# Optimization experiments

Hardware: AMD Instinct MI355X
Metric: run time of the kernel (lower is better)

## Reference

```python
import jax, jax.numpy as jnp
import numpy as np

NUM_HEADS = 8
NUM_CLS = 1
WINDOW = 4          # one-sided window radius
DILATION = 2
THETA = 10000.0
COORD_HIGH = 100000.0


def _rotate_half(t):
    # [..., x1, x2, ...] -> [..., -x2, x1, ...]
    x1 = t[..., 0::2]
    x2 = t[..., 1::2]
    return jnp.stack([-x2, x1], axis=-1).reshape(t.shape)


def _rope2d(t, coords):
    # t: (B, H, L, D), coords: (B, L, 2)
    head_dim = t.shape[-1]
    half = head_dim // 2
    inv_freq = 1.0 / (THETA ** (jnp.arange(0, half, 2, dtype=jnp.float32) / half))  # (half//2,)
    xy = coords.astype(jnp.float32) / COORD_HIGH                                    # (B, L, 2)
    fx = xy[..., 0][..., None] * inv_freq                                           # (B, L, half//2)
    fy = xy[..., 1][..., None] * inv_freq
    fx = jnp.repeat(fx, 2, axis=-1)                                                 # (B, L, half)
    fy = jnp.repeat(fy, 2, axis=-1)
    freqs = jnp.concatenate([fx, fy], axis=-1)                                      # (B, L, D)
    cos = jnp.cos(freqs)[:, None]                                                   # (B, 1, L, D)
    sin = jnp.sin(freqs)[:, None]
    return t * cos + _rotate_half(t) * sin


def setup_inputs() -> dict:
    key = jax.random.key(0)
    k1, k2, k3, k4 = jax.random.split(key, 4)
    B, L, E = 2, 8192, 512
    S = NUM_CLS + L
    x = jax.random.normal(k1, (B, S, E), dtype=jnp.float32)
    coords = jax.random.randint(k2, (B, L, 2), 0, 100000, dtype=jnp.int32)
    w_qkv = jax.random.normal(k3, (3 * E, E), dtype=jnp.float32) * 0.02
    b_qkv = jnp.zeros((3 * E,), dtype=jnp.float32)
    w_out = jax.random.normal(k4, (E, E), dtype=jnp.float32) * 0.02
    b_out = jnp.zeros((E,), dtype=jnp.float32)
    return {"x": x, "coords": coords, "w_qkv": w_qkv, "b_qkv": b_qkv,
            "w_out": w_out, "b_out": b_out}


def reference(x, coords, w_qkv, b_qkv, w_out, b_out):
    B, S, E = x.shape
    H = NUM_HEADS
    D = E // H
    L = S - NUM_CLS
    scale = 1.0 / np.sqrt(D).astype(np.float32)

    qkv = x @ w_qkv.T + b_qkv                                  # (B, S, 3E)
    qkv = qkv.reshape(B, S, 3, H, D).transpose(2, 0, 3, 1, 4)  # (3, B, H, S, D)
    q, k, v = qkv[0], qkv[1], qkv[2]

    # 2D RoPE on patch tokens only
    q = jnp.concatenate([q[:, :, :NUM_CLS], _rope2d(q[:, :, NUM_CLS:], coords)], axis=2)
    k = jnp.concatenate([k[:, :, :NUM_CLS], _rope2d(k[:, :, NUM_CLS:], coords)], axis=2)

    # ---- global CLS queries attend to all tokens ----
    s_cls = jnp.einsum('bhqd,bhkd->bhqk', q[:, :, :NUM_CLS], k) * scale
    cls_out = jnp.einsum('bhqk,bhkd->bhqd', jax.nn.softmax(s_cls, axis=-1), v)

    # ---- patch queries: CLS keys + dilated local window ----
    q_p = q[:, :, NUM_CLS:]
    k_p, v_p = k[:, :, NUM_CLS:], v[:, :, NUM_CLS:]
    k_cls, v_cls = k[:, :, :NUM_CLS], v[:, :, :NUM_CLS]

    pad = WINDOW * DILATION
    W = 2 * WINDOW + 1
    kp = jnp.pad(k_p, ((0, 0), (0, 0), (pad, pad), (0, 0)))
    vp = jnp.pad(v_p, ((0, 0), (0, 0), (pad, pad), (0, 0)))

    pos = jnp.arange(L)
    offsets = jnp.arange(W) * DILATION
    gidx = pos[:, None] + offsets[None, :]                     # (L, W), indices into padded seq
    kw = jnp.take(kp, gidx, axis=2)                            # (B, H, L, W, D)
    vw = jnp.take(vp, gidx, axis=2)

    win_pos = (jnp.arange(W) - WINDOW) * DILATION
    in_bounds = (pos[:, None] + win_pos >= 0) & (pos[:, None] + win_pos < L)  # (L, W)

    s_win = jnp.einsum('bhld,bhlwd->bhlw', q_p, kw) * scale
    s_win = jnp.where(in_bounds, s_win, -jnp.inf)
    s_c = jnp.einsum('bhld,bhcd->bhlc', q_p, k_cls) * scale
    attn = jax.nn.softmax(jnp.concatenate([s_c, s_win], axis=-1), axis=-1)  # (B,H,L,C+W)

    patch_out = (jnp.einsum('bhlc,bhcd->bhld', attn[..., :NUM_CLS], v_cls)
                 + jnp.einsum('bhlw,bhlwd->bhld', attn[..., NUM_CLS:], vw))

    out = jnp.concatenate([cls_out, patch_out], axis=2)        # (B, H, S, D)
    out = out.transpose(0, 2, 1, 3).reshape(B, S, E)
    return out @ w_out.T + b_out
```

## Files before the change

### kernel.cpp

```cpp
#include <hip/hip_runtime.h>
#include <math.h>

#define B_ 2
#define S_ 8193
#define L_ 8192
#define E_ 512
#define H_ 8
#define D_ 64
#define QKV_COLS 1536
#define SCALE 0.125f
#define M_ROWS 16386
#define M_PAD 16512

typedef unsigned short u16;
typedef __attribute__((ext_vector_type(8))) short bf16x8;
typedef __attribute__((ext_vector_type(8))) unsigned short u16x8;
typedef __attribute__((ext_vector_type(4))) float f32x4;

__device__ __forceinline__ u16 f2bf(float f) {
    unsigned u = __float_as_uint(f);
    unsigned r = (u + 0x7fffu + ((u >> 16) & 1u)) >> 16;
    return (u16)r;
}
__device__ __forceinline__ float bf2f(u16 h) {
    return __uint_as_float((unsigned)h << 16);
}

__device__ __forceinline__ void gload_lds16(const void* g, void* l) {
    __builtin_amdgcn_global_load_lds(
        (const __attribute__((address_space(1))) void*)g,
        (__attribute__((address_space(3))) void*)l, 16, 0, 0);
}

#define WAITV0() asm volatile("s_waitcnt vmcnt(0)" ::: "memory")
#define BAR()    __builtin_amdgcn_s_barrier()

#define PREP_W0 (M_PAD * E_ / 4)
#define PREP_W1 (QKV_COLS * E_ / 4)
#define PREP_W2 (E_ * E_ / 4)
#define PREP_W3 (B_ * L_ * 32)
#define PREP_W4 ((M_PAD - M_ROWS) * E_ / 8)
#define PREP_TOTAL (PREP_W0 + PREP_W1 + PREP_W2 + PREP_W3 + PREP_W4)

__global__ __launch_bounds__(256) void prep_kernel(
    const float* __restrict__ x,
    const float* __restrict__ w_qkv, const float* __restrict__ w_out,
    const int* __restrict__ coords,
    u16* __restrict__ xb, u16* __restrict__ wqb, u16* __restrict__ wob,
    float2* __restrict__ tab, u16* __restrict__ attnb)
{
    long i = (long)blockIdx.x * 256 + threadIdx.x;
    if (i < PREP_W0) {
        const long row = i >> 7;
        ushort4 o = make_ushort4(0, 0, 0, 0);
        if (row < M_ROWS) {
            const float4 v = *(const float4*)(x + i * 4);
            o.x = f2bf(v.x); o.y = f2bf(v.y); o.z = f2bf(v.z); o.w = f2bf(v.w);
        }
        *(ushort4*)(xb + i * 4) = o;
        return;
    }
    i -= PREP_W0;
    if (i < PREP_W1) {
        const float4 v = *(const float4*)(w_qkv + i * 4);
        ushort4 o = { f2bf(v.x), f2bf(v.y), f2bf(v.z), f2bf(v.w) };
        *(ushort4*)(wqb + i * 4) = o;
        return;
    }
    i -= PREP_W1;
    if (i < PREP_W2) {
        const float4 v = *(const float4*)(w_out + i * 4);
        ushort4 o = { f2bf(v.x), f2bf(v.y), f2bf(v.z), f2bf(v.w) };
        *(ushort4*)(wob + i * 4) = o;
        return;
    }
    i -= PREP_W2;
    if (i < PREP_W3) {
        const int p2 = (int)i & 31;
        const int bl = (int)i >> 5;
        const float coord = (float)coords[(size_t)bl * 2 + (p2 >> 4)] * 1e-5f;
        const float inv = exp2f(-0.83048202372184f * (float)(p2 & 15));
        float sn, cs;
        __sincosf(coord * inv, &sn, &cs);
        tab[i] = make_float2(cs, sn);
        return;
    }
    i -= PREP_W3;
    if (i < PREP_W4) {
        u16x8 z = {};
        *(u16x8*)(attnb + (size_t)M_ROWS * E_ + i * 8) = z;
    }
}

template <int MODE>
__global__ __launch_bounds__(512, 6) void gemm512(
    const u16* __restrict__ A, const u16* __restrict__ W,
    const float* __restrict__ bias, void* __restrict__ Cv,
    const float2* __restrict__ tab, int M, int N)
{
    __shared__ __align__(16) u16 smem[16384];

    const int nwg = gridDim.x * gridDim.y;
    const int orig = blockIdx.y * gridDim.x + blockIdx.x;
    const int qq = nwg >> 3, rr = nwg & 7;
    const int xcd = orig & 7, off = orig >> 3;
    const int wgid = (xcd < rr ? xcd * (qq + 1) : rr * (qq + 1) + (xcd - rr) * qq) + off;
    const int m0 = (wgid / gridDim.x) * 128;
    const int n0 = (wgid % gridDim.x) * 128;

    const int tid  = threadIdx.x;
    const int wid  = tid >> 6;
    const int lane = tid & 63;
    const int wm = (wid >> 2) * 64;
    const int wn = (wid & 3) * 32;
    const int fr = lane & 15;
    const int fq = lane >> 4;
    const int sfq = (fq ^ ((fr >> 1) & 3)) * 8;

    const int arow = tid >> 2;
    const int agch = ((tid & 3) ^ ((arow >> 1) & 3)) * 8;
    const u16* ga = A + (size_t)(m0 + arow) * 512 + agch;
    const u16* gw = W + (size_t)(n0 + arow) * 512 + agch;

    f32x4 acc[4][2] = {};

    #define STAGE(rb, kt)                                                       \
        do {                                                                    \
            gload_lds16(ga + (kt) * 32, smem + (rb) * 4096 + wid * 512);        \
            gload_lds16(gw + (kt) * 32, smem + 8192 + (rb) * 4096 + wid * 512); \
        } while (0)

    #define COMPUTE(rb)                                                         \
        do {                                                                    \
            const u16* as_ = smem + (rb) * 4096;                                \
            const u16* bs_ = smem + 8192 + (rb) * 4096;                         \
            bf16x8 a[4], b[2];                                                  \
            _Pragma("unroll")                                                   \
            for (int mi = 0; mi < 4; ++mi)                                      \
                a[mi] = *(const bf16x8*)(as_ + (wm + mi * 16 + fr) * 32 + sfq); \
            _Pragma("unroll")                                                   \
            for (int ni = 0; ni < 2; ++ni)                                      \
                b[ni] = *(const bf16x8*)(bs_ + (wn + ni * 16 + fr) * 32 + sfq); \
            _Pragma("unroll")                                                   \
            for (int mi = 0; mi < 4; ++mi)                                      \
                _Pragma("unroll")                                               \
                for (int ni = 0; ni < 2; ++ni)                                  \
                    acc[mi][ni] = __builtin_amdgcn_mfma_f32_16x16x32_bf16(      \
                        a[mi], b[ni], acc[mi][ni], 0, 0, 0);                    \
        } while (0)

    STAGE(0, 0);

    for (int t = 0; t < 16; ++t) {
        WAITV0();
        BAR();
        if (t + 1 < 16) STAGE((t + 1) & 1, t + 1);
        COMPUTE(t & 1);
    }

    #undef STAGE
    #undef COMPUTE

    __syncthreads();

    if (MODE == 1) {
        u16* st = smem;
        const bool rope_blk = (n0 < 2 * E_);
        #pragma unroll
        for (int mi = 0; mi < 4; ++mi) {
            #pragma unroll
            for (int j = 0; j < 4; ++j) {
                const int row = wm + mi * 16 + fq * 4 + j;
                const int gm = m0 + row;
                int b = 0, s = gm;
                if (gm >= S_) { b = 1; s = gm - S_; }
                const bool rot = rope_blk && (gm < M) && (s > 0);
                const float2* trow = tab + ((size_t)(b * L_ + (s - 1)) << 5);
                #pragma unroll
                for (int ni = 0; ni < 2; ++ni) {
                    const int col = wn + ni * 16 + fr;
                    const int gn = n0 + col;
                    float v = acc[mi][ni][j] + bias[gn];
                    const float partner = __shfl_xor(v, 1, 64);
                    if (rot) {
                        const float2 tt = trow[(gn & 63) >> 1];
                        v = (gn & 1) ? (v * tt.x + partner * tt.y)
                                     : (v * tt.x - partner * tt.y);
                    }
                    st[row * 128 + col] = f2bf(v);
                }
            }
        }
        __syncthreads();
        u16* C = (u16*)Cv;
        #pragma unroll
        for (int i = 0; i < 4; ++i) {
            const int slot = i * 512 + tid;
            const int row = slot >> 4;
            const int coff = (slot & 15) * 8;
            const int gm = m0 + row;
            if (gm < M)
                *(u16x8*)(C + (size_t)gm * N + n0 + coff) =
                    *(const u16x8*)(st + row * 128 + coff);
        }
    } else {
        float* stf = (float*)smem;
        float* C = (float*)Cv;
        #pragma unroll
        for (int h = 0; h < 2; ++h) {
            if ((wid >> 2) == h) {
                #pragma unroll
                for (int mi = 0; mi < 4; ++mi)
                    #pragma unroll
                    for (int j = 0; j < 4; ++j) {
                        const int lrow = mi * 16 + fq * 4 + j;
                        #pragma unroll
                        for (int ni = 0; ni < 2; ++ni) {
                            const int col = wn + ni * 16 + fr;
                            stf[lrow * 128 + col] = acc[mi][ni][j] + bias[n0 + col];
                        }
                    }
            }
            __syncthreads();
            #pragma unroll
            for (int i = 0; i < 4; ++i) {
                const int slot = i * 512 + tid;
                const int row = slot >> 5;
                const int coff = (slot & 31) * 4;
                const int gm = m0 + h * 64 + row;
                if (gm < M)
                    *(float4*)(C + (size_t)gm * N + n0 + coff) =
                        *(const float4*)(stf + row * 128 + coff);
            }
            __syncthreads();
        }
    }
}

#define NCHUNK 64
#define CLS_ROWS 129
#define CLS_BLOCKS (B_ * H_ * NCHUNK)
#define PQT 256
#define PATCH_BLOCKS (B_ * H_ * (L_ / PQT))

__global__ __launch_bounds__(256) void attn_fused(
    const u16* __restrict__ qkvb, float* __restrict__ part,
    u16* __restrict__ attnb)
{
    __shared__ __align__(16) u16 sbuf[272 * 64];
    __shared__ float kcvc[128];
    __shared__ float sm4[4], sl4[4];

    const int blk = blockIdx.x;

    if (blk < CLS_BLOCKS) {
        const int bh = blk >> 6, ch = blk & 63;
        const int b = bh >> 3, h = bh & 7;
        const int wid = threadIdx.x >> 6, lane = threadIdx.x & 63;
        const size_t base = (size_t)b * S_ * QKV_COLS;

        const float q = bf2f(qkvb[base + h * D_ + lane]);

        const int lo = ch * CLS_ROWS;
        const int hi = (lo + CLS_ROWS < S_) ? lo + CLS_ROWS : S_;

        float m = -1e30f, lsum = 0.f, acc = 0.f;
        for (int j = lo + wid; j < hi; j += 4) {
            const size_t roff = base + (size_t)j * QKV_COLS;
            float t = q * bf2f(qkvb[roff + E_ + h * D_ + lane]);
            #pragma unroll
            for (int o = 32; o; o >>= 1) t += __shfl_xor(t, o, 64);
            t *= SCALE;
            const float mn = fmaxf(m, t);
            const float corr = __expf(m - mn);
            const float p = __expf(t - mn);
            lsum = lsum * corr + p;
            acc = acc * corr + p * bf2f(qkvb[roff + 2 * E_ + h * D_ + lane]);
            m = mn;
        }

        float* sacc = (float*)sbuf;
        if (lane == 0) { sm4[wid] = m; sl4[wid] = lsum; }
        sacc[wid * 64 + lane] = acc;
        __syncthreads();
        if (wid == 0) {
            const float gm = fmaxf(fmaxf(sm4[0], sm4[1]), fmaxf(sm4[2], sm4[3]));
            float gl = 0.f, ga = 0.f;
            #pragma unroll
            for (int w = 0; w < 4; ++w) {
                const float c = __expf(sm4[w] - gm);
                gl += sl4[w] * c;
                ga += sacc[w * 64 + lane] * c;
            }
            float* pp = part + ((size_t)bh * NCHUNK + ch) * 66;
            if (lane == 0) { pp[0] = gm; pp[1] = gl; }
            pp[2 + lane] = ga;
        }
        return;
    }

    const int pblk = blk - CLS_BLOCKS;
    const int qt = pblk & 31;
    const int h = (pblk >> 5) & 7;
    const int b = pblk >> 8;
    const int l0 = qt * PQT;
    const size_t base = (size_t)b * S_ * QKV_COLS;
    const int hoff = h * D_;

    u16* kv = sbuf;
    float* kc = kcvc;
    float* vc = kcvc + 64;

    const int t = threadIdx.x;

    if (t < 64) kc[t] = bf2f(qkvb[base + E_ + hoff + t]);
    else if (t < 128) vc[t - 64] = bf2f(qkvb[base + 2 * E_ + hoff + (t - 64)]);

    #pragma unroll
    for (int i = 0; i < 9; ++i) {
        const int s = i * 256 + t;
        if (s < 272 * 8) {
            const int r = s >> 3, c = s & 7;
            const int lg = l0 - 8 + r;
            u16x8 v = {};
            if (lg >= 0 && lg < L_)
                v = *(const u16x8*)(qkvb + base + (size_t)(1 + lg) * QKV_COLS + E_ + hoff + c * 8);
            *(u16x8*)(kv + r * 64 + ((c ^ (r & 7)) * 8)) = v;
        }
    }
    __syncthreads();

    const int l = l0 + t;
    const size_t qrow = base + (size_t)(1 + l) * QKV_COLS + hoff;

    float s[10];
    #pragma unroll
    for (int w = 0; w < 10; ++w) s[w] = 0.f;

    #pragma unroll
    for (int c = 0; c < 8; ++c) {
        const u16x8 qv = *(const u16x8*)(qkvb + qrow + c * 8);
        float qf[8];
        #pragma unroll
        for (int i = 0; i < 8; ++i) qf[i] = bf2f(qv[i]);
        #pragma unroll
        for (int i = 0; i < 8; ++i) s[0] += qf[i] * kc[c * 8 + i];
        #pragma unroll
        for (int w = 0; w < 9; ++w) {
            const int kr = t + 2 * w;
            const u16x8 kk = *(const u16x8*)(kv + kr * 64 + ((c ^ (kr & 7)) * 8));
            #pragma unroll
            for (int i = 0; i < 8; ++i) s[1 + w] += qf[i] * bf2f(kk[i]);
        }
    }

    s[0] *= SCALE;
    #pragma unroll
    for (int w = 0; w < 9; ++w) {
        const int lp = l + 2 * w - 8;
        s[1 + w] = (lp >= 0 && lp < L_) ? s[1 + w] * SCALE : -1e30f;
    }
    float m = s[0];
    #pragma unroll
    for (int w = 1; w < 10; ++w) m = fmaxf(m, s[w]);
    float sum = 0.f;
    #pragma unroll
    for (int w = 0; w < 10; ++w) { s[w] = __expf(s[w] - m); sum += s[w]; }
    const float rsum = 1.0f / sum;

    __syncthreads();
    #pragma unroll
    for (int i = 0; i < 9; ++i) {
        const int sl = i * 256 + t;
        if (sl < 272 * 8) {
            const int r = sl >> 3, c = sl & 7;
            const int lg = l0 - 8 + r;
            u16x8 v = {};
            if (lg >= 0 && lg < L_)
                v = *(const u16x8*)(qkvb + base + (size_t)(1 + lg) * QKV_COLS + 2 * E_ + hoff + c * 8);
            *(u16x8*)(kv + r * 64 + ((c ^ (r & 7)) * 8)) = v;
        }
    }
    __syncthreads();

    const size_t orow = (size_t)(b * S_ + 1 + l) * E_ + hoff;
    #pragma unroll
    for (int c = 0; c < 8; ++c) {
        float acc[8];
        #pragma unroll
        for (int i = 0; i < 8; ++i) acc[i] = s[0] * vc[c * 8 + i];
        #pragma unroll
        for (int w = 0; w < 9; ++w) {
            const int vr = t + 2 * w;
            const u16x8 vv = *(const u16x8*)(kv + vr * 64 + ((c ^ (vr & 7)) * 8));
            #pragma unroll
            for (int i = 0; i < 8; ++i) acc[i] += s[1 + w] * bf2f(vv[i]);
        }
        u16x8 o;
        #pragma unroll
        for (int i = 0; i < 8; ++i) o[i] = f2bf(acc[i] * rsum);
        *(u16x8*)(attnb + orow + c * 8) = o;
    }
}

__global__ __launch_bounds__(64) void cls_attn_stage2(
    const float* __restrict__ part, u16* __restrict__ attnb)
{
    const int bh = blockIdx.x;
    const int lane = threadIdx.x;
    const int b = bh >> 3, h = bh & 7;
    float gm = -1e30f;
    for (int c = 0; c < NCHUNK; ++c)
        gm = fmaxf(gm, part[((size_t)bh * NCHUNK + c) * 66]);
    float gl = 0.f, ga = 0.f;
    for (int c = 0; c < NCHUNK; ++c) {
        const float* pp = part + ((size_t)bh * NCHUNK + c) * 66;
        const float w = __expf(pp[0] - gm);
        gl += pp[1] * w;
        ga += pp[2 + lane] * w;
    }
    attnb[(size_t)(b * S_) * E_ + h * D_ + lane] = f2bf(ga / gl);
}

extern "C" void kernel_launch(void* const* d_in, const int* in_sizes, int n_in,
                              void* d_out, int out_size, void* d_ws, size_t ws_size,
                              hipStream_t stream)
{
    const float* x      = (const float*)d_in[0];
    const int*   coords = (const int*)  d_in[1];
    const float* w_qkv  = (const float*)d_in[2];
    const float* b_qkv  = (const float*)d_in[3];
    const float* w_out  = (const float*)d_in[4];
    const float* b_out  = (const float*)d_in[5];
    float* out = (float*)d_out;

    u16*   qkvb  = (u16*)d_ws;
    u16*   attnb = qkvb + (size_t)M_ROWS * QKV_COLS;
    u16*   xb    = attnb + (size_t)M_PAD * E_;
    u16*   wqb   = xb + (size_t)M_PAD * E_;
    u16*   wob   = wqb + (size_t)QKV_COLS * E_;
    float* part  = (float*)(wob + (size_t)E_ * E_);
    float2* tab  = (float2*)(part + (size_t)16 * NCHUNK * 66);

    prep_kernel<<<(PREP_TOTAL + 255) / 256, 256, 0, stream>>>(
        x, w_qkv, w_out, coords, xb, wqb, wob, tab, attnb);

    {
        dim3 grid(QKV_COLS / 128, M_PAD / 128);
        gemm512<1><<<grid, 512, 0, stream>>>(
            xb, wqb, b_qkv, qkvb, tab, M_ROWS, QKV_COLS);
    }

    attn_fused<<<CLS_BLOCKS + PATCH_BLOCKS, 256, 0, stream>>>(qkvb, part, attnb);

    cls_attn_stage2<<<B_ * H_, 64, 0, stream>>>(part, attnb);

    {
        dim3 grid(E_ / 128, M_PAD / 128);
        gemm512<0><<<grid, 512, 0, stream>>>(
            attnb, wob, b_out, out, nullptr, M_ROWS, E_);
    }
}
```

Measured before the change: 135.1 us.

## Restructure CLS attention to tile 256 keys per block through shared memory

The CLS-token attention pass now has each block stage 256 K rows in swizzled LDS. It computes one score per thread, does a block-wide max and sum reduction, then stages V and accumulates the weighted sum. This replaces the serial per-row online softmax, which used shuffle reductions and scalar global loads per key, and reduces the chunk count from 64 to 33. The trade is extra block barriers and tree reductions, and fewer CLS blocks in the launch.

```diff
diff --git a/kernel.cpp b/kernel.cpp
--- a/kernel.cpp
+++ b/kernel.cpp
@@ -237,11 +237,11 @@
     }
 }
 
-#define NCHUNK 64
-#define CLS_ROWS 129
-#define CLS_BLOCKS (B_ * H_ * NCHUNK)
+#define NCHUNK2 33
+#define CLS_BLOCKS (B_ * H_ * NCHUNK2)
 #define PQT 256
 #define PATCH_BLOCKS (B_ * H_ * (L_ / PQT))
+#define PART_STRIDE ((size_t)16 * 64 * 66)
 
 __global__ __launch_bounds__(256) void attn_fused(
     const u16* __restrict__ qkvb, float* __restrict__ part,
@@ -249,51 +249,91 @@
 {
     __shared__ __align__(16) u16 sbuf[272 * 64];
     __shared__ float kcvc[128];
-    __shared__ float sm4[4], sl4[4];
+    __shared__ float red[256];
+    __shared__ float esh[256];
 
     const int blk = blockIdx.x;
+    const int t = threadIdx.x;
 
     if (blk < CLS_BLOCKS) {
-        const int bh = blk >> 6, ch = blk & 63;
+        const int bh = blk / NCHUNK2, ch = blk % NCHUNK2;
         const int b = bh >> 3, h = bh & 7;
-        const int wid = threadIdx.x >> 6, lane = threadIdx.x & 63;
         const size_t base = (size_t)b * S_ * QKV_COLS;
-
-        const float q = bf2f(qkvb[base + h * D_ + lane]);
-
-        const int lo = ch * CLS_ROWS;
-        const int hi = (lo + CLS_ROWS < S_) ? lo + CLS_ROWS : S_;
-
-        float m = -1e30f, lsum = 0.f, acc = 0.f;
-        for (int j = lo + wid; j < hi; j += 4) {
-            const size_t roff = base + (size_t)j * QKV_COLS;
-            float t = q * bf2f(qkvb[roff + E_ + h * D_ + lane]);
+        const int hoff = h * D_;
+        const int lo = ch * 256;
+        const int wid = t >> 6, lane = t & 63;
+
+        u16* kv = sbuf;
+        float* qs = kcvc;
+
+        if (t < 64) qs[t] = bf2f(qkvb[base + hoff + t]);
+
+        #pragma unroll
+        for (int i = 0; i < 8; ++i) {
+            const int s2 = i * 256 + t;
+            const int r = s2 >> 3, c = s2 & 7;
+            const int gr = lo + r;
+            u16x8 v = {};
+            if (gr < S_)
+                v = *(const u16x8*)(qkvb + base + (size_t)gr * QKV_COLS + E_ + hoff + c * 8);
+            *(u16x8*)(kv + r * 64 + ((c ^ (r & 7)) * 8)) = v;
+        }
+        __syncthreads();
+
+        const bool valid = (lo + t) < S_;
+        float sval = 0.f;
+        #pragma unroll
+        for (int c = 0; c < 8; ++c) {
+            const u16x8 kk = *(const u16x8*)(kv + t * 64 + ((c ^ (t & 7)) * 8));
             #pragma unroll
-            for (int o = 32; o; o >>= 1) t += __shfl_xor(t, o, 64);
-            t *= SCALE;
-            const float mn = fmaxf(m, t);
-            const float corr = __expf(m - mn);
-            const float p = __expf(t - mn);
-            lsum = lsum * corr + p;
-            acc = acc * corr + p * bf2f(qkvb[roff + 2 * E_ + h * D_ + lane]);
-            m = mn;
-        }
-
-        float* sacc = (float*)sbuf;
-        if (lane == 0) { sm4[wid] = m; sl4[wid] = lsum; }
-        sacc[wid * 64 + lane] = acc;
+            for (int i = 0; i < 8; ++i) sval += qs[c * 8 + i] * bf2f(kk[i]);
+        }
+        sval = valid ? sval * SCALE : -1e30f;
+
+        red[t] = sval;
+        __syncthreads();
+        for (int o = 128; o; o >>= 1) {
+            if (t < o) red[t] = fmaxf(red[t], red[t + o]);
+            __syncthreads();
+        }
+        const float m = red[0];
+        __syncthreads();
+
+        const float e = valid ? __expf(sval - m) : 0.f;
+        esh[t] = e;
+        red[t] = e;
+        __syncthreads();
+        for (int o = 128; o; o >>= 1) {
+            if (t < o) red[t] += red[t + o];
+            __syncthreads();
+        }
+        const float lsum = red[0];
+
+        __syncthreads();
+        #pragma unroll
+        for (int i = 0; i < 8; ++i) {
+            const int s2 = i * 256 + t;
+            const int r = s2 >> 3, c = s2 & 7;
+            const int gr = lo + r;
+            u16x8 v = {};
+            if (gr < S_)
+                v = *(const u16x8*)(qkvb + base + (size_t)gr * QKV_COLS + 2 * E_ + hoff + c * 8);
+            *(u16x8*)(kv + r * 64 + ((c ^ (r & 7)) * 8)) = v;
+        }
+        __syncthreads();
+
+        float acc = 0.f;
+        for (int j64 = 0; j64 < 64; ++j64) {
+            const int j = (wid << 6) + j64;
+            const float ej = esh[j];
+            acc += ej * bf2f(kv[j * 64 + (((lane >> 3) ^ (j & 7)) * 8) + (lane & 7)]);
+        }
+        red[t] = acc;
         __syncthreads();
         if (wid == 0) {
-            const float gm = fmaxf(fmaxf(sm4[0], sm4[1]), fmaxf(sm4[2], sm4[3]));
-            float gl = 0.f, ga = 0.f;
-            #pragma unroll
-            for (int w = 0; w < 4; ++w) {
-                const float c = __expf(sm4[w] - gm);
-                gl += sl4[w] * c;
-                ga += sacc[w * 64 + lane] * c;
-            }
-            float* pp = part + ((size_t)bh * NCHUNK + ch) * 66;
-            if (lane == 0) { pp[0] = gm; pp[1] = gl; }
+            const float ga = red[lane] + red[64 + lane] + red[128 + lane] + red[192 + lane];
+            float* pp = part + ((size_t)bh * NCHUNK2 + ch) * 66;
+            if (lane == 0) { pp[0] = m; pp[1] = lsum; }
             pp[2 + lane] = ga;
         }
         return;
@@ -310,8 +350,6 @@
     u16* kv = sbuf;
     float* kc = kcvc;
     float* vc = kcvc + 64;
-
-    const int t = threadIdx.x;
 
     if (t < 64) kc[t] = bf2f(qkvb[base + E_ + hoff + t]);
     else if (t < 128) vc[t - 64] = bf2f(qkvb[base + 2 * E_ + hoff + (t - 64)]);
@@ -410,11 +448,11 @@
     const int lane = threadIdx.x;
     const int b = bh >> 3, h = bh & 7;
     float gm = -1e30f;
-    for (int c = 0; c < NCHUNK; ++c)
-        gm = fmaxf(gm, part[((size_t)bh * NCHUNK + c) * 66]);
+    for (int c = 0; c < NCHUNK2; ++c)
+        gm = fmaxf(gm, part[((size_t)bh * NCHUNK2 + c) * 66]);
     float gl = 0.f, ga = 0.f;
-    for (int c = 0; c < NCHUNK; ++c) {
-        const float* pp = part + ((size_t)bh * NCHUNK + c) * 66;
+    for (int c = 0; c < NCHUNK2; ++c) {
+        const float* pp = part + ((size_t)bh * NCHUNK2 + c) * 66;
         const float w = __expf(pp[0] - gm);
         gl += pp[1] * w;
         ga += pp[2 + lane] * w;
@@ -440,7 +478,7 @@
     u16*   wqb   = xb + (size_t)M_PAD * E_;
     u16*   wob   = wqb + (size_t)QKV_COLS * E_;
     float* part  = (float*)(wob + (size_t)E_ * E_);
-    float2* tab  = (float2*)(part + (size_t)16 * NCHUNK * 66);
+    float2* tab  = (float2*)(part + PART_STRIDE);
 
     prep_kernel<<<(PREP_TOTAL + 255) / 256, 256, 0, stream>>>(
         x, w_qkv, w_out, coords, xb, wqb, wob, tab, attnb);
```

Result: faster. 120.0 us (-11.1%).
